# Kernel optimization log

Hardware: AMD Instinct MI355X
Metric: run time of the kernel (lower is better)

## Reference

```python
import jax, jax.numpy as jnp
import numpy as np

SOS = 1

def _gru_cell(x, h, Wih, Whh, bih, bhh):
    # PyTorch GRU cell: gates ordered (r, z, n)
    gi = x @ Wih.T + bih
    gh = h @ Whh.T + bhh
    ir, iz, inn = jnp.split(gi, 3, axis=-1)
    hr, hz, hn = jnp.split(gh, 3, axis=-1)
    r = jax.nn.sigmoid(ir + hr)
    z = jax.nn.sigmoid(iz + hz)
    n = jnp.tanh(inn + r * hn)
    return (1.0 - z) * n + z * h


def setup_inputs() -> dict:
    key = jax.random.key(0)
    ks = jax.random.split(key, 17)
    V, E, H, Lin, Tout, B, Lmax = 50000, 512, 512, 400, 100, 64, 400
    s = 0.05
    f = jax.random.normal
    return {
        "emb":     f(ks[0], (V, E)) * s,
        "enc_Wih": f(ks[1], (3 * H, E)) * s,
        "enc_Whh": f(ks[2], (3 * H, H)) * s,
        "enc_bih": f(ks[3], (3 * H,)) * s,
        "enc_bhh": f(ks[4], (3 * H,)) * s,
        "attn_W":  f(ks[5], (Lmax, 2 * H)) * s,
        "attn_b":  f(ks[6], (Lmax,)) * s,
        "comb_W":  f(ks[7], (H, 2 * H)) * s,
        "comb_b":  f(ks[8], (H,)) * s,
        "dec_Wih": f(ks[9], (3 * H, H)) * s,
        "dec_Whh": f(ks[10], (3 * H, H)) * s,
        "dec_bih": f(ks[11], (3 * H,)) * s,
        "dec_bhh": f(ks[12], (3 * H,)) * s,
        "out_W":   f(ks[13], (V, H)) * s,
        "out_b":   f(ks[14], (V,)) * s,
        "input_tensor":  jax.random.randint(ks[15], (Lin, B), 0, V),
        "target_tensor": jax.random.randint(ks[16], (Tout, B), 0, V),
    }


def reference(emb, enc_Wih, enc_Whh, enc_bih, enc_bhh, attn_W, attn_b,
              comb_W, comb_b, dec_Wih, dec_Whh, dec_bih, dec_bhh,
              out_W, out_b, input_tensor, target_tensor):
    B = input_tensor.shape[1]
    H = enc_Whh.shape[1]

    # ---- encoder: 1-layer GRU over [L, B, E] ----
    enc_x = emb[input_tensor]                      # [L, B, E]
    h0 = jnp.zeros((B, H), enc_x.dtype)
    def enc_step(h, x):
        h2 = _gru_cell(x, h, enc_Wih, enc_Whh, enc_bih, enc_bhh)
        return h2, h2
    h_enc, enc_out = jax.lax.scan(enc_step, h0, enc_x)   # enc_out: [L, B, H]
    enc0 = enc_out[0]                              # [B, H]; source's attn_applied[0] picks timestep 0

    # ---- decoder: teacher-forced, NLLLoss(mean) summed over steps ----
    dec_tokens = jnp.concatenate(
        [jnp.full((1, B), SOS, target_tensor.dtype), target_tensor[:-1]], axis=0)
    dec_x = emb[dec_tokens]                        # [T, B, H] (embed_size == hidden_size)

    def dec_step(h, xt):
        x, tgt = xt                                # x: [B, H], tgt: [B]
        a = jax.nn.softmax(jnp.concatenate([x, h], 1) @ attn_W.T + attn_b, axis=1)  # [B, Lmax]
        # faithful to source: elementwise broadcast picks enc_out[0] scaled by a[:, 0]
        ctx = enc0 * a[:, :1]                      # [B, H]
        c = jax.nn.relu(jnp.concatenate([x, ctx], 1) @ comb_W.T + comb_b)           # [B, H]
        h2 = _gru_cell(c, h, dec_Wih, dec_Whh, dec_bih, dec_bhh)
        logp = jax.nn.log_softmax(h2 @ out_W.T + out_b, axis=1)                     # [B, V]
        loss_t = -jnp.mean(jnp.take_along_axis(logp, tgt[:, None], axis=1))
        return h2, loss_t

    _, losses = jax.lax.scan(dec_step, h_enc, (dec_x, target_tensor))
    return jnp.sum(losses)
```

## Files before the change

### kernel.cpp

```cpp
#include <hip/hip_runtime.h>
#include <math.h>


typedef __attribute__((ext_vector_type(8))) short bh8;
typedef __attribute__((ext_vector_type(4))) float fv4;

__device__ __forceinline__ float b2f(short u) {
    union { unsigned int i; float f; } c;
    c.i = ((unsigned int)(unsigned short)u) << 16;
    return c.f;
}
__device__ __forceinline__ short f2b(float f) {
    union { float f; unsigned int u; } c;
    c.f = f;
    unsigned int r = (c.u + 0x7fffu + ((c.u >> 16) & 1u)) >> 16;
    return (short)r;
}
__device__ __forceinline__ bh8 ld8(const float* __restrict__ p) {
    bh8 r;
    #pragma unroll
    for (int j = 0; j < 8; ++j) r[j] = f2b(p[j]);
    return r;
}
__device__ __forceinline__ float sigmf(float x) { return 1.f / (1.f + expf(-x)); }

__device__ __forceinline__ fv4 mfma16(bh8 a, bh8 b, fv4 c) {
    return __builtin_amdgcn_mfma_f32_16x16x32_bf16(a, b, c, 0, 0, 0);
}

__device__ __forceinline__ void gridbar(unsigned int* bar, unsigned int target) {
    __syncthreads();
    if (threadIdx.x == 0) {
        __hip_atomic_fetch_add(bar, 1u, __ATOMIC_ACQ_REL, __HIP_MEMORY_SCOPE_AGENT);
        while (__hip_atomic_load(bar, __ATOMIC_ACQUIRE, __HIP_MEMORY_SCOPE_AGENT) < target) {
            __builtin_amdgcn_s_sleep(2);
        }
    }
    __syncthreads();
}

__global__ __launch_bounds__(256) void k_cvt(
    const float* __restrict__ s, short* __restrict__ d, int n)
{
    const int i = (blockIdx.x * 256 + threadIdx.x) * 4;
    if (i + 3 < n) {
        fv4 v = *(const fv4*)(s + i);
        short4 o;
        o.x = f2b(v[0]); o.y = f2b(v[1]); o.z = f2b(v[2]); o.w = f2b(v[3]);
        *(short4*)(d + i) = o;
    }
}

__global__ __launch_bounds__(256) void k_enc_persist(
    const float* __restrict__ emb, const int* __restrict__ input_t,
    const short* __restrict__ Wb,
    const float* __restrict__ Wih_f, const float* __restrict__ Whh_f,
    const float* __restrict__ bih, const float* __restrict__ bhh,
    float* __restrict__ h_f32, short* __restrict__ h_bf,
    float* __restrict__ enc0, unsigned int* __restrict__ bar)
{
    const int tid  = threadIdx.x;
    const int lane = tid & 63;
    const int wv   = tid >> 6;
    const int n0   = blockIdx.x * 16;
    const int b0   = wv * 16;
    const int l15  = lane & 15;
    const int ko   = lane >> 4;
    const int koff = ko * 8;
    const int brow = b0 + l15;
    const int n    = n0 + l15;

    for (int i = blockIdx.x * 256 + tid; i < 64 * 512; i += 32 * 256) {
        h_f32[i] = 0.f; h_bf[i] = 0;
    }
    gridbar(bar, 32u);

    const bh8 *Wrb = nullptr, *Wzb = nullptr, *Wnb = nullptr;
    const bh8 *Urb = nullptr, *Uzb = nullptr, *Unb = nullptr;
    const float *Wrf = nullptr, *Wzf = nullptr, *Wnf = nullptr;
    const float *Urf = nullptr, *Uzf = nullptr, *Unf = nullptr;
    if (Wb) {
        Wrb = (const bh8*)(Wb + (long long)(n + 0)    * 512) + ko;
        Wzb = (const bh8*)(Wb + (long long)(n + 512)  * 512) + ko;
        Wnb = (const bh8*)(Wb + (long long)(n + 1024) * 512) + ko;
        Urb = (const bh8*)(Wb + (long long)(n + 1536) * 512) + ko;
        Uzb = (const bh8*)(Wb + (long long)(n + 2048) * 512) + ko;
        Unb = (const bh8*)(Wb + (long long)(n + 2560) * 512) + ko;
    } else {
        Wrf = Wih_f + (long long)(n + 0)    * 512 + koff;
        Wzf = Wih_f + (long long)(n + 512)  * 512 + koff;
        Wnf = Wih_f + (long long)(n + 1024) * 512 + koff;
        Urf = Whh_f + (long long)(n + 0)    * 512 + koff;
        Uzf = Whh_f + (long long)(n + 512)  * 512 + koff;
        Unf = Whh_f + (long long)(n + 1024) * 512 + koff;
    }
    const float bir = bih[n], biz = bih[n + 512], bin = bih[n + 1024];
    const float bhr = bhh[n], bhz = bhh[n + 512], bhn = bhh[n + 1024];

    for (int t = 0; t < 400; ++t) {
        const float* hi  = h_f32 + (t & 1) * 32768;
        const short* hib = h_bf  + (t & 1) * 32768;
        float* ho  = h_f32 + ((t + 1) & 1) * 32768;
        short* hob = h_bf  + ((t + 1) & 1) * 32768;

        const int tok = input_t[t * 64 + brow];
        const float* Ap = emb + (long long)tok * 512 + koff;
        const bh8*  Hp  = (const bh8*)(hib + (long long)brow * 512) + ko;

        fv4 air = {0.f, 0.f, 0.f, 0.f};
        fv4 aiz = air, ain = air, ahr = air, ahz = air, ahn = air;
        if (Wb) {
            #pragma unroll 4
            for (int kk = 0; kk < 16; ++kk) {
                const bh8 a = ld8(Ap + kk * 32);
                const bh8 h = Hp[kk * 4];
                air = mfma16(a, Wrb[kk * 4], air);
                aiz = mfma16(a, Wzb[kk * 4], aiz);
                ain = mfma16(a, Wnb[kk * 4], ain);
                ahr = mfma16(h, Urb[kk * 4], ahr);
                ahz = mfma16(h, Uzb[kk * 4], ahz);
                ahn = mfma16(h, Unb[kk * 4], ahn);
            }
        } else {
            #pragma unroll 4
            for (int kk = 0; kk < 16; ++kk) {
                const bh8 a = ld8(Ap + kk * 32);
                const bh8 h = Hp[kk * 4];
                air = mfma16(a, ld8(Wrf + kk * 32), air);
                aiz = mfma16(a, ld8(Wzf + kk * 32), aiz);
                ain = mfma16(a, ld8(Wnf + kk * 32), ain);
                ahr = mfma16(h, ld8(Urf + kk * 32), ahr);
                ahz = mfma16(h, ld8(Uzf + kk * 32), ahz);
                ahn = mfma16(h, ld8(Unf + kk * 32), ahn);
            }
        }
        #pragma unroll
        for (int r = 0; r < 4; ++r) {
            const int b = b0 + ko * 4 + r;
            const float rr = sigmf(air[r] + bir + ahr[r] + bhr);
            const float zz = sigmf(aiz[r] + biz + ahz[r] + bhz);
            const float nn = tanhf(ain[r] + bin + rr * (ahn[r] + bhn));
            const float hold = hi[b * 512 + n];
            const float hnew = (1.f - zz) * nn + zz * hold;
            ho[b * 512 + n] = hnew;
            hob[b * 512 + n] = f2b(hnew);
            if (t == 0) enc0[b * 512 + n] = hnew;
        }
        gridbar(bar, 32u * (t + 2));
    }
}

__global__ __launch_bounds__(256) void k_gru1(
    const short* __restrict__ c_bf, const short* __restrict__ Wb,
    const float* __restrict__ Wih_f, const float* __restrict__ Whh_f,
    const float* __restrict__ bih, const float* __restrict__ bhh,
    const float* __restrict__ hi, const short* __restrict__ hib,
    float* __restrict__ ho, short* __restrict__ hob)
{
    const int tid  = threadIdx.x;
    const int lane = tid & 63;
    const int w    = blockIdx.x * 4 + (tid >> 6);
    const int b0   = (w & 3) * 16;
    const int n0   = (w >> 2) * 16;
    const int l15  = lane & 15;
    const int ko   = lane >> 4;
    const int koff = ko * 8;
    const int brow = b0 + l15;
    const int n    = n0 + l15;

    const bh8* Ap = (const bh8*)(c_bf + (long long)brow * 512) + ko;
    const bh8* Hp = (const bh8*)(hib + (long long)brow * 512) + ko;

    fv4 air = {0.f, 0.f, 0.f, 0.f};
    fv4 aiz = air, ain = air, ahr = air, ahz = air, ahn = air;
    if (Wb) {
        const bh8* Wr = (const bh8*)(Wb + (long long)(n + 0)    * 512) + ko;
        const bh8* Wz = (const bh8*)(Wb + (long long)(n + 512)  * 512) + ko;
        const bh8* Wn = (const bh8*)(Wb + (long long)(n + 1024) * 512) + ko;
        const bh8* Ur = (const bh8*)(Wb + (long long)(n + 1536) * 512) + ko;
        const bh8* Uz = (const bh8*)(Wb + (long long)(n + 2048) * 512) + ko;
        const bh8* Un = (const bh8*)(Wb + (long long)(n + 2560) * 512) + ko;
        #pragma unroll 4
        for (int kk = 0; kk < 16; ++kk) {
            const bh8 a = Ap[kk * 4];
            const bh8 h = Hp[kk * 4];
            air = mfma16(a, Wr[kk * 4], air);
            aiz = mfma16(a, Wz[kk * 4], aiz);
            ain = mfma16(a, Wn[kk * 4], ain);
            ahr = mfma16(h, Ur[kk * 4], ahr);
            ahz = mfma16(h, Uz[kk * 4], ahz);
            ahn = mfma16(h, Un[kk * 4], ahn);
        }
    } else {
        const float* Wr = Wih_f + (long long)(n + 0)    * 512 + koff;
        const float* Wz = Wih_f + (long long)(n + 512)  * 512 + koff;
        const float* Wn = Wih_f + (long long)(n + 1024) * 512 + koff;
        const float* Ur = Whh_f + (long long)(n + 0)    * 512 + koff;
        const float* Uz = Whh_f + (long long)(n + 512)  * 512 + koff;
        const float* Un = Whh_f + (long long)(n + 1024) * 512 + koff;
        #pragma unroll 4
        for (int kk = 0; kk < 16; ++kk) {
            const bh8 a = Ap[kk * 4];
            const bh8 h = Hp[kk * 4];
            air = mfma16(a, ld8(Wr + kk * 32), air);
            aiz = mfma16(a, ld8(Wz + kk * 32), aiz);
            ain = mfma16(a, ld8(Wn + kk * 32), ain);
            ahr = mfma16(h, ld8(Ur + kk * 32), ahr);
            ahz = mfma16(h, ld8(Uz + kk * 32), ahz);
            ahn = mfma16(h, ld8(Un + kk * 32), ahn);
        }
    }
    const float bir = bih[n], biz = bih[n + 512], bin = bih[n + 1024];
    const float bhr = bhh[n], bhz = bhh[n + 512], bhn = bhh[n + 1024];
    #pragma unroll
    for (int r = 0; r < 4; ++r) {
        const int b = b0 + ko * 4 + r;
        const float rr = sigmf(air[r] + bir + ahr[r] + bhr);
        const float zz = sigmf(aiz[r] + biz + ahz[r] + bhz);
        const float nn = tanhf(ain[r] + bin + rr * (ahn[r] + bhn));
        const float hold = hi[b * 512 + n];
        const float hnew = (1.f - zz) * nn + zz * hold;
        ho[b * 512 + n] = hnew;
        hob[b * 512 + n] = f2b(hnew);
    }
}

__global__ __launch_bounds__(256) void k_attncomb(
    const float* __restrict__ emb, const float* __restrict__ h_f32,
    const float* __restrict__ enc0,
    const float* __restrict__ attn_W, const float* __restrict__ attn_b,
    const float* __restrict__ comb_W, const float* __restrict__ comb_b,
    const int* __restrict__ target, int td, short* __restrict__ c_bf)
{
    __shared__ float sx[1024];
    __shared__ float sc[400];
    __shared__ float red[256];
    __shared__ float a0s;
    const int b = blockIdx.x;
    const int tid = threadIdx.x;
    const int tok = (td == 0) ? 1 : target[(td - 1) * 64 + b];
    for (int k = tid; k < 512; k += 256) {
        sx[k] = emb[(long long)tok * 512 + k];
        sx[512 + k] = h_f32[b * 512 + k];
    }
    __syncthreads();
    for (int nn = tid; nn < 400; nn += 256) {
        const fv4* wrow = (const fv4*)(attn_W + (long long)nn * 1024);
        float acc = 0.f;
        for (int kc = 0; kc < 256; ++kc) {
            fv4 v = wrow[kc];
            acc += v[0] * sx[kc * 4 + 0] + v[1] * sx[kc * 4 + 1]
                 + v[2] * sx[kc * 4 + 2] + v[3] * sx[kc * 4 + 3];
        }
        sc[nn] = acc + attn_b[nn];
    }
    __syncthreads();
    float m = -1e30f;
    for (int nn = tid; nn < 400; nn += 256) m = fmaxf(m, sc[nn]);
    red[tid] = m;
    __syncthreads();
    for (int s = 128; s > 0; s >>= 1) {
        if (tid < s) red[tid] = fmaxf(red[tid], red[tid + s]);
        __syncthreads();
    }
    m = red[0];
    __syncthreads();
    float ss = 0.f;
    for (int nn = tid; nn < 400; nn += 256) ss += expf(sc[nn] - m);
    red[tid] = ss;
    __syncthreads();
    for (int s = 128; s > 0; s >>= 1) {
        if (tid < s) red[tid] += red[tid + s];
        __syncthreads();
    }
    if (tid == 0) a0s = expf(sc[0] - m) / red[0];
    __syncthreads();
    const float a0b = a0s;
    for (int k = tid; k < 512; k += 256) sx[512 + k] = enc0[b * 512 + k] * a0b;
    __syncthreads();
    for (int j = tid; j < 512; j += 256) {
        const fv4* wrow = (const fv4*)(comb_W + (long long)j * 1024);
        float acc = 0.f;
        for (int kc = 0; kc < 256; ++kc) {
            fv4 v = wrow[kc];
            acc += v[0] * sx[kc * 4 + 0] + v[1] * sx[kc * 4 + 1]
                 + v[2] * sx[kc * 4 + 2] + v[3] * sx[kc * 4 + 3];
        }
        acc += comb_b[j];
        c_bf[b * 512 + j] = f2b(fmaxf(acc, 0.f));
    }
}

__global__ __launch_bounds__(256) void k_outloss(
    const short* __restrict__ h2bf,
    const short* __restrict__ outWb, const float* __restrict__ outW,
    const float* __restrict__ outb, const int* __restrict__ target,
    float* __restrict__ pm, float* __restrict__ ps, float* __restrict__ tlogit)
{
    __shared__ float sl[64][65];
    const int tid  = threadIdx.x;
    const int lane = tid & 63;
    const int wl   = tid >> 6;
    const int base = blockIdx.x * 64;
    const int n0   = base + wl * 16;
    const int l15  = lane & 15;
    const int ko   = lane >> 4;

    const int v    = n0 + l15;
    const int vcl  = (v < 50000) ? v : 49999;
    const bh8* A0 = (const bh8*)(h2bf + (long long)(0  + l15) * 512) + ko;
    const bh8* A1 = (const bh8*)(h2bf + (long long)(16 + l15) * 512) + ko;
    const bh8* A2 = (const bh8*)(h2bf + (long long)(32 + l15) * 512) + ko;
    const bh8* A3 = (const bh8*)(h2bf + (long long)(48 + l15) * 512) + ko;
    fv4 c0 = {0.f, 0.f, 0.f, 0.f};
    fv4 c1 = c0, c2 = c0, c3 = c0;
    if (outWb) {
        const bh8* Bp = (const bh8*)(outWb + (long long)vcl * 512) + ko;
        #pragma unroll 4
        for (int kk = 0; kk < 16; ++kk) {
            const bh8 bb = Bp[kk * 4];
            c0 = mfma16(A0[kk * 4], bb, c0);
            c1 = mfma16(A1[kk * 4], bb, c1);
            c2 = mfma16(A2[kk * 4], bb, c2);
            c3 = mfma16(A3[kk * 4], bb, c3);
        }
    } else {
        const float* Bp = outW + (long long)vcl * 512 + ko * 8;
        #pragma unroll 4
        for (int kk = 0; kk < 16; ++kk) {
            const bh8 bb = ld8(Bp + kk * 32);
            c0 = mfma16(A0[kk * 4], bb, c0);
            c1 = mfma16(A1[kk * 4], bb, c1);
            c2 = mfma16(A2[kk * 4], bb, c2);
            c3 = mfma16(A3[kk * 4], bb, c3);
        }
    }
    const float bv = outb[vcl];
    const int cc = wl * 16 + l15;
    const bool ok = (v < 50000);
    #pragma unroll
    for (int r = 0; r < 4; ++r) {
        const int row = ko * 4 + r;
        sl[0  + row][cc] = ok ? (c0[r] + bv) : -1e30f;
        sl[16 + row][cc] = ok ? (c1[r] + bv) : -1e30f;
        sl[32 + row][cc] = ok ? (c2[r] + bv) : -1e30f;
        sl[48 + row][cc] = ok ? (c3[r] + bv) : -1e30f;
    }
    __syncthreads();
    if (tid < 64) {
        const int b = tid;
        float m = -1e30f, s = 0.f;
        for (int c = 0; c < 64; ++c) {
            const float x = sl[b][c];
            if (x > m) { s = s * expf(m - x) + 1.f; m = x; }
            else       { s += expf(x - m); }
        }
        pm[blockIdx.x * 64 + b] = m;
        ps[blockIdx.x * 64 + b] = s;
        const int tg = target[b];
        const int rel = tg - base;
        if (rel >= 0 && rel < 64) tlogit[b] = sl[b][rel];
    }
}

__global__ __launch_bounds__(256) void k_lossred(
    const float* __restrict__ pm, const float* __restrict__ ps,
    const float* __restrict__ tlogit, float* __restrict__ loss_acc)
{
    __shared__ float rm[256], rs[256];
    const int b = blockIdx.x;
    const int tid = threadIdx.x;
    float m = -1e30f, s = 0.f;
    for (int i = tid; i < 782; i += 256) {
        const float m2 = pm[i * 64 + b];
        const float s2 = ps[i * 64 + b];
        if (m2 > m) { s = s * expf(m - m2) + s2; m = m2; }
        else        { s += s2 * expf(m2 - m); }
    }
    rm[tid] = m; rs[tid] = s;
    __syncthreads();
    for (int st = 128; st > 0; st >>= 1) {
        if (tid < st) {
            const float m2 = rm[tid + st], s2 = rs[tid + st];
            const float M = fmaxf(rm[tid], m2);
            rs[tid] = rs[tid] * expf(rm[tid] - M) + s2 * expf(m2 - M);
            rm[tid] = M;
        }
        __syncthreads();
    }
    if (tid == 0) {
        const float logp = tlogit[b] - (rm[0] + logf(rs[0]));
        atomicAdd(loss_acc, -logp * (1.f / 64.f));
    }
}

__global__ void k_init(float* h_f32_0, short* h_bf_0, float* loss_acc,
                       unsigned int* bar)
{
    const int i = blockIdx.x * 256 + threadIdx.x;
    if (i < 64 * 512) { h_f32_0[i] = 0.f; h_bf_0[i] = 0; }
    if (i == 0) { *loss_acc = 0.f; *bar = 0u; }
}

__global__ void k_final(const float* loss_acc, float* out)
{
    out[0] = *loss_acc;
}

extern "C" void kernel_launch(void* const* d_in, const int* in_sizes, int n_in,
                              void* d_out, int out_size, void* d_ws, size_t ws_size,
                              hipStream_t stream)
{
    const float* emb     = (const float*)d_in[0];
    const float* enc_Wih = (const float*)d_in[1];
    const float* enc_Whh = (const float*)d_in[2];
    const float* enc_bih = (const float*)d_in[3];
    const float* enc_bhh = (const float*)d_in[4];
    const float* attn_W  = (const float*)d_in[5];
    const float* attn_b  = (const float*)d_in[6];
    const float* comb_W  = (const float*)d_in[7];
    const float* comb_b  = (const float*)d_in[8];
    const float* dec_Wih = (const float*)d_in[9];
    const float* dec_Whh = (const float*)d_in[10];
    const float* dec_bih = (const float*)d_in[11];
    const float* dec_bhh = (const float*)d_in[12];
    const float* out_W   = (const float*)d_in[13];
    const float* out_b   = (const float*)d_in[14];
    const int*   input_t = (const int*)d_in[15];
    const int*   target_t= (const int*)d_in[16];

    char* ws = (char*)d_ws;
    float* h_f32  = (float*)(ws + 0);
    float* enc0   = (float*)(ws + 262144);
    short* h_bf   = (short*)(ws + 393216);
    short* c_bf   = (short*)(ws + 524288);
    float* lacc   = (float*)(ws + 589824);
    unsigned int* bar = (unsigned int*)(ws + 590080);
    float* pm     = (float*)(ws + 590336);
    float* ps     = (float*)(ws + 790528);
    float* tlog   = (float*)(ws + 990720);
    short* encWb  = (short*)(ws + 990976);
    short* decWb  = (short*)(ws + 4136704);
    short* outWb  = (short*)(ws + 7282432);

    const bool tier1 = ws_size >= 7282432;
    const bool tier2 = ws_size >= 58482432;

    k_init<<<128, 256, 0, stream>>>(h_f32, h_bf, lacc, bar);

    if (tier1) {
        k_cvt<<<768, 256, 0, stream>>>(enc_Wih, encWb, 786432);
        k_cvt<<<768, 256, 0, stream>>>(enc_Whh, encWb + 786432, 786432);
        k_cvt<<<768, 256, 0, stream>>>(dec_Wih, decWb, 786432);
        k_cvt<<<768, 256, 0, stream>>>(dec_Whh, decWb + 786432, 786432);
    }
    if (tier2) {
        k_cvt<<<25000, 256, 0, stream>>>(out_W, outWb, 25600000);
    }

    k_enc_persist<<<32, 256, 0, stream>>>(
        emb, input_t, tier1 ? encWb : nullptr, enc_Wih, enc_Whh,
        enc_bih, enc_bhh, h_f32, h_bf, enc0, bar);

    for (int td = 0; td < 100; ++td) {
        const float* hi  = h_f32 + (td & 1) * 32768;
        const short* hib = h_bf  + (td & 1) * 32768;
        float* ho  = h_f32 + ((td + 1) & 1) * 32768;
        short* hob = h_bf  + ((td + 1) & 1) * 32768;
        k_attncomb<<<64, 256, 0, stream>>>(emb, hi, enc0, attn_W, attn_b,
                                           comb_W, comb_b, target_t, td, c_bf);
        k_gru1<<<32, 256, 0, stream>>>(c_bf, tier1 ? decWb : nullptr,
                                       dec_Wih, dec_Whh, dec_bih, dec_bhh,
                                       hi, hib, ho, hob);
        k_outloss<<<782, 256, 0, stream>>>(hob, tier2 ? outWb : nullptr, out_W,
                                           out_b, target_t + td * 64,
                                           pm, ps, tlog);
        k_lossred<<<64, 256, 0, stream>>>(pm, ps, tlog, lacc);
    }

    k_final<<<1, 1, 0, stream>>>(lacc, (float*)d_out);
}
```

Measured before the change: 28.92 ms.

## Fuse whole encoder-decoder pipeline into one persistent megakernel with grid barriers

Replaces the conversion kernels, the persistent encoder kernel and the roughly 400 per-step decoder kernel launches with a single 256-block persistent kernel. Stages are separated by software grid barriers: a dedicated barrier counter for the 32 encoder blocks and a global one for the other phases. The aim is to remove launch overhead and inter-kernel gaps across the 100 decoder steps. In exchange it relies on all 256 blocks being co-resident for the spin barriers and adds barrier latency on every phase.

```diff
diff --git a/kernel.cpp b/kernel.cpp
--- a/kernel.cpp
+++ b/kernel.cpp
@@ -5,14 +5,8 @@
 typedef __attribute__((ext_vector_type(8))) short bh8;
 typedef __attribute__((ext_vector_type(4))) float fv4;
 
-__device__ __forceinline__ float b2f(short u) {
-    union { unsigned int i; float f; } c;
-    c.i = ((unsigned int)(unsigned short)u) << 16;
-    return c.f;
-}
 __device__ __forceinline__ short f2b(float f) {
-    union { float f; unsigned int u; } c;
-    c.f = f;
+    union { float f; unsigned int u; } c; c.f = f;
     unsigned int r = (c.u + 0x7fffu + ((c.u >> 16) & 1u)) >> 16;
     return (short)r;
 }
@@ -23,388 +17,396 @@
     return r;
 }
 __device__ __forceinline__ float sigmf(float x) { return 1.f / (1.f + expf(-x)); }
-
 __device__ __forceinline__ fv4 mfma16(bh8 a, bh8 b, fv4 c) {
     return __builtin_amdgcn_mfma_f32_16x16x32_bf16(a, b, c, 0, 0, 0);
 }
 
-__device__ __forceinline__ void gridbar(unsigned int* bar, unsigned int target) {
+__device__ __forceinline__ void spinbar(unsigned int* bar, unsigned int target) {
     __syncthreads();
     if (threadIdx.x == 0) {
         __hip_atomic_fetch_add(bar, 1u, __ATOMIC_ACQ_REL, __HIP_MEMORY_SCOPE_AGENT);
-        while (__hip_atomic_load(bar, __ATOMIC_ACQUIRE, __HIP_MEMORY_SCOPE_AGENT) < target) {
+        while (__hip_atomic_load(bar, __ATOMIC_ACQUIRE, __HIP_MEMORY_SCOPE_AGENT) < target)
+            __builtin_amdgcn_s_sleep(8);
+    }
+    __syncthreads();
+}
+__device__ __forceinline__ void spinbar2(unsigned int* bar, unsigned int target) {
+    __syncthreads();
+    if (threadIdx.x == 0) {
+        __hip_atomic_fetch_add(bar, 1u, __ATOMIC_ACQ_REL, __HIP_MEMORY_SCOPE_AGENT);
+        while (__hip_atomic_load(bar, __ATOMIC_ACQUIRE, __HIP_MEMORY_SCOPE_AGENT) < target)
             __builtin_amdgcn_s_sleep(2);
-        }
     }
     __syncthreads();
 }
 
-__global__ __launch_bounds__(256) void k_cvt(
-    const float* __restrict__ s, short* __restrict__ d, int n)
-{
-    const int i = (blockIdx.x * 256 + threadIdx.x) * 4;
-    if (i + 3 < n) {
+__device__ __forceinline__ void cvtbuf(const float* __restrict__ s,
+                                       short* __restrict__ d, int n, int gtid) {
+    for (int i = gtid * 4; i < n; i += 65536 * 4) {
         fv4 v = *(const fv4*)(s + i);
-        short4 o;
-        o.x = f2b(v[0]); o.y = f2b(v[1]); o.z = f2b(v[2]); o.w = f2b(v[3]);
+        short4 o; o.x = f2b(v[0]); o.y = f2b(v[1]); o.z = f2b(v[2]); o.w = f2b(v[3]);
         *(short4*)(d + i) = o;
     }
 }
 
-__global__ __launch_bounds__(256) void k_enc_persist(
-    const float* __restrict__ emb, const int* __restrict__ input_t,
-    const short* __restrict__ Wb,
-    const float* __restrict__ Wih_f, const float* __restrict__ Whh_f,
-    const float* __restrict__ bih, const float* __restrict__ bhh,
+__global__ void k_init(float* lacc, unsigned int* gbar, unsigned int* ebar) {
+    *lacc = 0.f; *gbar = 0u; *ebar = 0u;
+}
+
+__global__ __launch_bounds__(256, 1) void k_mega(
+    const float* __restrict__ emb,
+    const float* __restrict__ encWih, const float* __restrict__ encWhh,
+    const float* __restrict__ encbih, const float* __restrict__ encbhh,
+    const float* __restrict__ attnW,  const float* __restrict__ attnb,
+    const float* __restrict__ combW,  const float* __restrict__ combb,
+    const float* __restrict__ decWih, const float* __restrict__ decWhh,
+    const float* __restrict__ decbih, const float* __restrict__ decbhh,
+    const float* __restrict__ outW,   const float* __restrict__ outb,
+    const int* __restrict__ input_t,  const int* __restrict__ target_t,
     float* __restrict__ h_f32, short* __restrict__ h_bf,
-    float* __restrict__ enc0, unsigned int* __restrict__ bar)
-{
-    const int tid  = threadIdx.x;
-    const int lane = tid & 63;
-    const int wv   = tid >> 6;
-    const int n0   = blockIdx.x * 16;
-    const int b0   = wv * 16;
-    const int l15  = lane & 15;
-    const int ko   = lane >> 4;
-    const int koff = ko * 8;
-    const int brow = b0 + l15;
-    const int n    = n0 + l15;
-
-    for (int i = blockIdx.x * 256 + tid; i < 64 * 512; i += 32 * 256) {
-        h_f32[i] = 0.f; h_bf[i] = 0;
-    }
-    gridbar(bar, 32u);
-
-    const bh8 *Wrb = nullptr, *Wzb = nullptr, *Wnb = nullptr;
-    const bh8 *Urb = nullptr, *Uzb = nullptr, *Unb = nullptr;
-    const float *Wrf = nullptr, *Wzf = nullptr, *Wnf = nullptr;
-    const float *Urf = nullptr, *Uzf = nullptr, *Unf = nullptr;
-    if (Wb) {
-        Wrb = (const bh8*)(Wb + (long long)(n + 0)    * 512) + ko;
-        Wzb = (const bh8*)(Wb + (long long)(n + 512)  * 512) + ko;
-        Wnb = (const bh8*)(Wb + (long long)(n + 1024) * 512) + ko;
-        Urb = (const bh8*)(Wb + (long long)(n + 1536) * 512) + ko;
-        Uzb = (const bh8*)(Wb + (long long)(n + 2048) * 512) + ko;
-        Unb = (const bh8*)(Wb + (long long)(n + 2560) * 512) + ko;
-    } else {
-        Wrf = Wih_f + (long long)(n + 0)    * 512 + koff;
-        Wzf = Wih_f + (long long)(n + 512)  * 512 + koff;
-        Wnf = Wih_f + (long long)(n + 1024) * 512 + koff;
-        Urf = Whh_f + (long long)(n + 0)    * 512 + koff;
-        Uzf = Whh_f + (long long)(n + 512)  * 512 + koff;
-        Unf = Whh_f + (long long)(n + 1024) * 512 + koff;
-    }
-    const float bir = bih[n], biz = bih[n + 512], bin = bih[n + 1024];
-    const float bhr = bhh[n], bhz = bhh[n + 512], bhn = bhh[n + 1024];
-
-    for (int t = 0; t < 400; ++t) {
-        const float* hi  = h_f32 + (t & 1) * 32768;
-        const short* hib = h_bf  + (t & 1) * 32768;
-        float* ho  = h_f32 + ((t + 1) & 1) * 32768;
-        short* hob = h_bf  + ((t + 1) & 1) * 32768;
-
-        const int tok = input_t[t * 64 + brow];
-        const float* Ap = emb + (long long)tok * 512 + koff;
-        const bh8*  Hp  = (const bh8*)(hib + (long long)brow * 512) + ko;
-
-        fv4 air = {0.f, 0.f, 0.f, 0.f};
-        fv4 aiz = air, ain = air, ahr = air, ahz = air, ahn = air;
-        if (Wb) {
-            #pragma unroll 4
-            for (int kk = 0; kk < 16; ++kk) {
-                const bh8 a = ld8(Ap + kk * 32);
-                const bh8 h = Hp[kk * 4];
-                air = mfma16(a, Wrb[kk * 4], air);
-                aiz = mfma16(a, Wzb[kk * 4], aiz);
-                ain = mfma16(a, Wnb[kk * 4], ain);
-                ahr = mfma16(h, Urb[kk * 4], ahr);
-                ahz = mfma16(h, Uzb[kk * 4], ahz);
-                ahn = mfma16(h, Unb[kk * 4], ahn);
-            }
-        } else {
-            #pragma unroll 4
-            for (int kk = 0; kk < 16; ++kk) {
-                const bh8 a = ld8(Ap + kk * 32);
-                const bh8 h = Hp[kk * 4];
-                air = mfma16(a, ld8(Wrf + kk * 32), air);
-                aiz = mfma16(a, ld8(Wzf + kk * 32), aiz);
-                ain = mfma16(a, ld8(Wnf + kk * 32), ain);
-                ahr = mfma16(h, ld8(Urf + kk * 32), ahr);
-                ahz = mfma16(h, ld8(Uzf + kk * 32), ahz);
-                ahn = mfma16(h, ld8(Unf + kk * 32), ahn);
-            }
-        }
-        #pragma unroll
-        for (int r = 0; r < 4; ++r) {
-            const int b = b0 + ko * 4 + r;
-            const float rr = sigmf(air[r] + bir + ahr[r] + bhr);
-            const float zz = sigmf(aiz[r] + biz + ahz[r] + bhz);
-            const float nn = tanhf(ain[r] + bin + rr * (ahn[r] + bhn));
-            const float hold = hi[b * 512 + n];
-            const float hnew = (1.f - zz) * nn + zz * hold;
-            ho[b * 512 + n] = hnew;
-            hob[b * 512 + n] = f2b(hnew);
-            if (t == 0) enc0[b * 512 + n] = hnew;
-        }
-        gridbar(bar, 32u * (t + 2));
-    }
-}
-
-__global__ __launch_bounds__(256) void k_gru1(
-    const short* __restrict__ c_bf, const short* __restrict__ Wb,
-    const float* __restrict__ Wih_f, const float* __restrict__ Whh_f,
-    const float* __restrict__ bih, const float* __restrict__ bhh,
-    const float* __restrict__ hi, const short* __restrict__ hib,
-    float* __restrict__ ho, short* __restrict__ hob)
-{
-    const int tid  = threadIdx.x;
-    const int lane = tid & 63;
-    const int w    = blockIdx.x * 4 + (tid >> 6);
-    const int b0   = (w & 3) * 16;
-    const int n0   = (w >> 2) * 16;
-    const int l15  = lane & 15;
-    const int ko   = lane >> 4;
-    const int koff = ko * 8;
-    const int brow = b0 + l15;
-    const int n    = n0 + l15;
-
-    const bh8* Ap = (const bh8*)(c_bf + (long long)brow * 512) + ko;
-    const bh8* Hp = (const bh8*)(hib + (long long)brow * 512) + ko;
-
-    fv4 air = {0.f, 0.f, 0.f, 0.f};
-    fv4 aiz = air, ain = air, ahr = air, ahz = air, ahn = air;
-    if (Wb) {
-        const bh8* Wr = (const bh8*)(Wb + (long long)(n + 0)    * 512) + ko;
-        const bh8* Wz = (const bh8*)(Wb + (long long)(n + 512)  * 512) + ko;
-        const bh8* Wn = (const bh8*)(Wb + (long long)(n + 1024) * 512) + ko;
-        const bh8* Ur = (const bh8*)(Wb + (long long)(n + 1536) * 512) + ko;
-        const bh8* Uz = (const bh8*)(Wb + (long long)(n + 2048) * 512) + ko;
-        const bh8* Un = (const bh8*)(Wb + (long long)(n + 2560) * 512) + ko;
-        #pragma unroll 4
-        for (int kk = 0; kk < 16; ++kk) {
-            const bh8 a = Ap[kk * 4];
-            const bh8 h = Hp[kk * 4];
-            air = mfma16(a, Wr[kk * 4], air);
-            aiz = mfma16(a, Wz[kk * 4], aiz);
-            ain = mfma16(a, Wn[kk * 4], ain);
-            ahr = mfma16(h, Ur[kk * 4], ahr);
-            ahz = mfma16(h, Uz[kk * 4], ahz);
-            ahn = mfma16(h, Un[kk * 4], ahn);
-        }
-    } else {
-        const float* Wr = Wih_f + (long long)(n + 0)    * 512 + koff;
-        const float* Wz = Wih_f + (long long)(n + 512)  * 512 + koff;
-        const float* Wn = Wih_f + (long long)(n + 1024) * 512 + koff;
-        const float* Ur = Whh_f + (long long)(n + 0)    * 512 + koff;
-        const float* Uz = Whh_f + (long long)(n + 512)  * 512 + koff;
-        const float* Un = Whh_f + (long long)(n + 1024) * 512 + koff;
-        #pragma unroll 4
-        for (int kk = 0; kk < 16; ++kk) {
-            const bh8 a = Ap[kk * 4];
-            const bh8 h = Hp[kk * 4];
-            air = mfma16(a, ld8(Wr + kk * 32), air);
-            aiz = mfma16(a, ld8(Wz + kk * 32), aiz);
-            ain = mfma16(a, ld8(Wn + kk * 32), ain);
-            ahr = mfma16(h, ld8(Ur + kk * 32), ahr);
-            ahz = mfma16(h, ld8(Uz + kk * 32), ahz);
-            ahn = mfma16(h, ld8(Un + kk * 32), ahn);
-        }
-    }
-    const float bir = bih[n], biz = bih[n + 512], bin = bih[n + 1024];
-    const float bhr = bhh[n], bhz = bhh[n + 512], bhn = bhh[n + 1024];
-    #pragma unroll
-    for (int r = 0; r < 4; ++r) {
-        const int b = b0 + ko * 4 + r;
-        const float rr = sigmf(air[r] + bir + ahr[r] + bhr);
-        const float zz = sigmf(aiz[r] + biz + ahz[r] + bhz);
-        const float nn = tanhf(ain[r] + bin + rr * (ahn[r] + bhn));
-        const float hold = hi[b * 512 + n];
-        const float hnew = (1.f - zz) * nn + zz * hold;
-        ho[b * 512 + n] = hnew;
-        hob[b * 512 + n] = f2b(hnew);
-    }
-}
-
-__global__ __launch_bounds__(256) void k_attncomb(
-    const float* __restrict__ emb, const float* __restrict__ h_f32,
-    const float* __restrict__ enc0,
-    const float* __restrict__ attn_W, const float* __restrict__ attn_b,
-    const float* __restrict__ comb_W, const float* __restrict__ comb_b,
-    const int* __restrict__ target, int td, short* __restrict__ c_bf)
+    float* __restrict__ enc0, short* __restrict__ c_bf,
+    float* __restrict__ pm, float* __restrict__ ps, float* __restrict__ tlog,
+    float* __restrict__ lacc, unsigned int* __restrict__ gbar,
+    unsigned int* __restrict__ ebar,
+    short* __restrict__ encWb, short* __restrict__ decWb,
+    short* __restrict__ outWb, int tier, float* __restrict__ outp)
 {
     __shared__ float sx[1024];
     __shared__ float sc[400];
     __shared__ float red[256];
+    __shared__ float rs2[256];
     __shared__ float a0s;
-    const int b = blockIdx.x;
+    __shared__ float sl[64][65];
+    __shared__ float sqm[256];
+    __shared__ float sqs[256];
+
+    const int bid = blockIdx.x;
     const int tid = threadIdx.x;
-    const int tok = (td == 0) ? 1 : target[(td - 1) * 64 + b];
-    for (int k = tid; k < 512; k += 256) {
-        sx[k] = emb[(long long)tok * 512 + k];
-        sx[512 + k] = h_f32[b * 512 + k];
-    }
-    __syncthreads();
-    for (int nn = tid; nn < 400; nn += 256) {
-        const fv4* wrow = (const fv4*)(attn_W + (long long)nn * 1024);
-        float acc = 0.f;
-        for (int kc = 0; kc < 256; ++kc) {
-            fv4 v = wrow[kc];
-            acc += v[0] * sx[kc * 4 + 0] + v[1] * sx[kc * 4 + 1]
-                 + v[2] * sx[kc * 4 + 2] + v[3] * sx[kc * 4 + 3];
-        }
-        sc[nn] = acc + attn_b[nn];
-    }
-    __syncthreads();
-    float m = -1e30f;
-    for (int nn = tid; nn < 400; nn += 256) m = fmaxf(m, sc[nn]);
-    red[tid] = m;
-    __syncthreads();
-    for (int s = 128; s > 0; s >>= 1) {
-        if (tid < s) red[tid] = fmaxf(red[tid], red[tid + s]);
+    const int gtid = bid * 256 + tid;
+    unsigned int gc = 0;
+
+    if (gtid < 32768) { h_f32[gtid] = 0.f; h_bf[gtid] = 0; }
+    if (tier >= 1) {
+        cvtbuf(encWih, encWb, 786432, gtid);
+        cvtbuf(encWhh, encWb + 786432, 786432, gtid);
+        cvtbuf(decWih, decWb, 786432, gtid);
+        cvtbuf(decWhh, decWb + 786432, 786432, gtid);
+    }
+    if (tier >= 2) cvtbuf(outW, outWb, 25600000, gtid);
+    gc += 256; spinbar(gbar, gc);
+
+    if (bid < 32) {
+        const int wv = tid >> 6, lane = tid & 63;
+        const int l15 = lane & 15, ko = lane >> 4, koff = ko * 8;
+        const int n0 = bid * 16, b0 = wv * 16;
+        const int brow = b0 + l15, n = n0 + l15;
+        const float bir = encbih[n], biz = encbih[n + 512], bin = encbih[n + 1024];
+        const float bhr = encbhh[n], bhz = encbhh[n + 512], bhn = encbhh[n + 1024];
+        unsigned int ec = 0;
+        #pragma unroll 1
+        for (int t = 0; t < 400; ++t) {
+            const float* hi  = h_f32 + (t & 1) * 32768;
+            const short* hib = h_bf  + (t & 1) * 32768;
+            float* ho  = h_f32 + ((t + 1) & 1) * 32768;
+            short* hob = h_bf  + ((t + 1) & 1) * 32768;
+            const int tok = input_t[t * 64 + brow];
+            const float* Ap = emb + (long long)tok * 512 + koff;
+            const bh8*  Hp  = (const bh8*)(hib + (long long)brow * 512) + ko;
+            fv4 air = {0.f, 0.f, 0.f, 0.f};
+            fv4 aiz = air, ain = air, ahr = air, ahz = air, ahn = air;
+            if (tier >= 1) {
+                const bh8* Wr = (const bh8*)(encWb + (long long)(n + 0)    * 512) + ko;
+                const bh8* Wz = (const bh8*)(encWb + (long long)(n + 512)  * 512) + ko;
+                const bh8* Wn = (const bh8*)(encWb + (long long)(n + 1024) * 512) + ko;
+                const bh8* Ur = (const bh8*)(encWb + (long long)(n + 1536) * 512) + ko;
+                const bh8* Uz = (const bh8*)(encWb + (long long)(n + 2048) * 512) + ko;
+                const bh8* Un = (const bh8*)(encWb + (long long)(n + 2560) * 512) + ko;
+                #pragma unroll 4
+                for (int kk = 0; kk < 16; ++kk) {
+                    const bh8 a = ld8(Ap + kk * 32);
+                    const bh8 h = Hp[kk * 4];
+                    air = mfma16(a, Wr[kk * 4], air);
+                    aiz = mfma16(a, Wz[kk * 4], aiz);
+                    ain = mfma16(a, Wn[kk * 4], ain);
+                    ahr = mfma16(h, Ur[kk * 4], ahr);
+                    ahz = mfma16(h, Uz[kk * 4], ahz);
+                    ahn = mfma16(h, Un[kk * 4], ahn);
+                }
+            } else {
+                const float* Wr = encWih + (long long)(n + 0)    * 512 + koff;
+                const float* Wz = encWih + (long long)(n + 512)  * 512 + koff;
+                const float* Wn = encWih + (long long)(n + 1024) * 512 + koff;
+                const float* Ur = encWhh + (long long)(n + 0)    * 512 + koff;
+                const float* Uz = encWhh + (long long)(n + 512)  * 512 + koff;
+                const float* Un = encWhh + (long long)(n + 1024) * 512 + koff;
+                #pragma unroll 4
+                for (int kk = 0; kk < 16; ++kk) {
+                    const bh8 a = ld8(Ap + kk * 32);
+                    const bh8 h = Hp[kk * 4];
+                    air = mfma16(a, ld8(Wr + kk * 32), air);
+                    aiz = mfma16(a, ld8(Wz + kk * 32), aiz);
+                    ain = mfma16(a, ld8(Wn + kk * 32), ain);
+                    ahr = mfma16(h, ld8(Ur + kk * 32), ahr);
+                    ahz = mfma16(h, ld8(Uz + kk * 32), ahz);
+                    ahn = mfma16(h, ld8(Un + kk * 32), ahn);
+                }
+            }
+            #pragma unroll
+            for (int r = 0; r < 4; ++r) {
+                const int b = b0 + ko * 4 + r;
+                const float rr = sigmf(air[r] + bir + ahr[r] + bhr);
+                const float zz = sigmf(aiz[r] + biz + ahz[r] + bhz);
+                const float nn = tanhf(ain[r] + bin + rr * (ahn[r] + bhn));
+                const float hold = hi[b * 512 + n];
+                const float hnew = (1.f - zz) * nn + zz * hold;
+                ho[b * 512 + n] = hnew;
+                hob[b * 512 + n] = f2b(hnew);
+                if (t == 0) enc0[b * 512 + n] = hnew;
+            }
+            ec += 32; spinbar2(ebar, ec);
+        }
+    }
+    gc += 256; spinbar(gbar, gc);
+
+    #pragma unroll 1
+    for (int td = 0; td < 100; ++td) {
+        const float* hi  = h_f32 + (td & 1) * 32768;
+        const short* hib = h_bf  + (td & 1) * 32768;
+        float* ho  = h_f32 + ((td + 1) & 1) * 32768;
+        short* hob = h_bf  + ((td + 1) & 1) * 32768;
+
+        if (bid < 64) {
+            const int b = bid;
+            const int tok = (td == 0) ? 1 : target_t[(td - 1) * 64 + b];
+            for (int k = tid; k < 512; k += 256) {
+                sx[k] = emb[(long long)tok * 512 + k];
+                sx[512 + k] = hi[b * 512 + k];
+            }
+            __syncthreads();
+            for (int nn = tid; nn < 400; nn += 256) {
+                const fv4* wrow = (const fv4*)(attnW + (long long)nn * 1024);
+                float acc = 0.f;
+                for (int kc = 0; kc < 256; ++kc) {
+                    fv4 v = wrow[kc];
+                    acc += v[0] * sx[kc * 4 + 0] + v[1] * sx[kc * 4 + 1]
+                         + v[2] * sx[kc * 4 + 2] + v[3] * sx[kc * 4 + 3];
+                }
+                sc[nn] = acc + attnb[nn];
+            }
+            __syncthreads();
+            float m = -1e30f;
+            for (int nn = tid; nn < 400; nn += 256) m = fmaxf(m, sc[nn]);
+            red[tid] = m;
+            __syncthreads();
+            for (int s = 128; s > 0; s >>= 1) {
+                if (tid < s) red[tid] = fmaxf(red[tid], red[tid + s]);
+                __syncthreads();
+            }
+            m = red[0];
+            __syncthreads();
+            float ss = 0.f;
+            for (int nn = tid; nn < 400; nn += 256) ss += expf(sc[nn] - m);
+            red[tid] = ss;
+            __syncthreads();
+            for (int s = 128; s > 0; s >>= 1) {
+                if (tid < s) red[tid] += red[tid + s];
+                __syncthreads();
+            }
+            if (tid == 0) a0s = expf(sc[0] - m) / red[0];
+            __syncthreads();
+            const float a0b = a0s;
+            for (int k = tid; k < 512; k += 256)
+                sx[512 + k] = enc0[b * 512 + k] * a0b;
+            __syncthreads();
+            for (int j = tid; j < 512; j += 256) {
+                const fv4* wrow = (const fv4*)(combW + (long long)j * 1024);
+                float acc = 0.f;
+                for (int kc = 0; kc < 256; ++kc) {
+                    fv4 v = wrow[kc];
+                    acc += v[0] * sx[kc * 4 + 0] + v[1] * sx[kc * 4 + 1]
+                         + v[2] * sx[kc * 4 + 2] + v[3] * sx[kc * 4 + 3];
+                }
+                acc += combb[j];
+                c_bf[b * 512 + j] = f2b(fmaxf(acc, 0.f));
+            }
+        } else if (bid < 128 && td > 0) {
+            const int b = bid - 64;
+            red[tid] = pm[tid * 64 + b]; rs2[tid] = ps[tid * 64 + b];
+            __syncthreads();
+            for (int st = 128; st > 0; st >>= 1) {
+                if (tid < st) {
+                    const float m2 = red[tid + st], s2 = rs2[tid + st];
+                    const float M = fmaxf(red[tid], m2);
+                    rs2[tid] = rs2[tid] * expf(red[tid] - M) + s2 * expf(m2 - M);
+                    red[tid] = M;
+                }
+                __syncthreads();
+            }
+            if (tid == 0) {
+                const float logp = tlog[b] - (red[0] + logf(rs2[0]));
+                atomicAdd(lacc, -logp * (1.f / 64.f));
+            }
+        }
+        gc += 256; spinbar(gbar, gc);
+
+        if (bid < 32) {
+            const int lane = tid & 63;
+            const int w = bid * 4 + (tid >> 6);
+            const int b0 = (w & 3) * 16, n0 = (w >> 2) * 16;
+            const int l15 = lane & 15, ko = lane >> 4, koff = ko * 8;
+            const int brow = b0 + l15, n = n0 + l15;
+            const bh8* Ap = (const bh8*)(c_bf + (long long)brow * 512) + ko;
+            const bh8* Hp = (const bh8*)(hib + (long long)brow * 512) + ko;
+            fv4 air = {0.f, 0.f, 0.f, 0.f};
+            fv4 aiz = air, ain = air, ahr = air, ahz = air, ahn = air;
+            if (tier >= 1) {
+                const bh8* Wr = (const bh8*)(decWb + (long long)(n + 0)    * 512) + ko;
+                const bh8* Wz = (const bh8*)(decWb + (long long)(n + 512)  * 512) + ko;
+                const bh8* Wn = (const bh8*)(decWb + (long long)(n + 1024) * 512) + ko;
+                const bh8* Ur = (const bh8*)(decWb + (long long)(n + 1536) * 512) + ko;
+                const bh8* Uz = (const bh8*)(decWb + (long long)(n + 2048) * 512) + ko;
+                const bh8* Un = (const bh8*)(decWb + (long long)(n + 2560) * 512) + ko;
+                #pragma unroll 4
+                for (int kk = 0; kk < 16; ++kk) {
+                    const bh8 a = Ap[kk * 4];
+                    const bh8 h = Hp[kk * 4];
+                    air = mfma16(a, Wr[kk * 4], air);
+                    aiz = mfma16(a, Wz[kk * 4], aiz);
+                    ain = mfma16(a, Wn[kk * 4], ain);
+                    ahr = mfma16(h, Ur[kk * 4], ahr);
+                    ahz = mfma16(h, Uz[kk * 4], ahz);
+                    ahn = mfma16(h, Un[kk * 4], ahn);
+                }
+            } else {
+                const float* Wr = decWih + (long long)(n + 0)    * 512 + koff;
+                const float* Wz = decWih + (long long)(n + 512)  * 512 + koff;
+                const float* Wn = decWih + (long long)(n + 1024) * 512 + koff;
+                const float* Ur = decWhh + (long long)(n + 0)    * 512 + koff;
+                const float* Uz = decWhh + (long long)(n + 512)  * 512 + koff;
+                const float* Un = decWhh + (long long)(n + 1024) * 512 + koff;
+                #pragma unroll 4
+                for (int kk = 0; kk < 16; ++kk) {
+                    const bh8 a = Ap[kk * 4];
+                    const bh8 h = Hp[kk * 4];
+                    air = mfma16(a, ld8(Wr + kk * 32), air);
+                    aiz = mfma16(a, ld8(Wz + kk * 32), aiz);
+                    ain = mfma16(a, ld8(Wn + kk * 32), ain);
+                    ahr = mfma16(h, ld8(Ur + kk * 32), ahr);
+                    ahz = mfma16(h, ld8(Uz + kk * 32), ahz);
+                    ahn = mfma16(h, ld8(Un + kk * 32), ahn);
+                }
+            }
+            const float bir = decbih[n], biz = decbih[n + 512], bin = decbih[n + 1024];
+            const float bhr = decbhh[n], bhz = decbhh[n + 512], bhn = decbhh[n + 1024];
+            #pragma unroll
+            for (int r = 0; r < 4; ++r) {
+                const int b = b0 + ko * 4 + r;
+                const float rr = sigmf(air[r] + bir + ahr[r] + bhr);
+                const float zz = sigmf(aiz[r] + biz + ahz[r] + bhz);
+                const float nn = tanhf(ain[r] + bin + rr * (ahn[r] + bhn));
+                const float hold = hi[b * 512 + n];
+                const float hnew = (1.f - zz) * nn + zz * hold;
+                ho[b * 512 + n] = hnew;
+                hob[b * 512 + n] = f2b(hnew);
+            }
+        }
+        gc += 256; spinbar(gbar, gc);
+
+        {
+            const int wl = tid >> 6, lane = tid & 63;
+            const int l15 = lane & 15, ko = lane >> 4;
+            const bh8* A0 = (const bh8*)(hob + (long long)(0  + l15) * 512) + ko;
+            const bh8* A1 = (const bh8*)(hob + (long long)(16 + l15) * 512) + ko;
+            const bh8* A2 = (const bh8*)(hob + (long long)(32 + l15) * 512) + ko;
+            const bh8* A3 = (const bh8*)(hob + (long long)(48 + l15) * 512) + ko;
+            const int row = tid & 63, q = tid >> 6;
+            const int tg = target_t[td * 64 + row];
+            float qm = -1e30f, qs = 0.f;
+            #pragma unroll 1
+            for (int j = 0; j < 4; ++j) {
+                const int strip = bid * 4 + wl + 1024 * j;
+                const int v = strip * 16 + l15;
+                const int vcl = (v < 50000) ? v : 49999;
+                fv4 c0 = {0.f, 0.f, 0.f, 0.f};
+                fv4 c1 = c0, c2 = c0, c3 = c0;
+                if (tier >= 2) {
+                    const bh8* Bp = (const bh8*)(outWb + (long long)vcl * 512) + ko;
+                    #pragma unroll 4
+                    for (int kk = 0; kk < 16; ++kk) {
+                        const bh8 bb = Bp[kk * 4];
+                        c0 = mfma16(A0[kk * 4], bb, c0);
+                        c1 = mfma16(A1[kk * 4], bb, c1);
+                        c2 = mfma16(A2[kk * 4], bb, c2);
+                        c3 = mfma16(A3[kk * 4], bb, c3);
+                    }
+                } else {
+                    const float* Bp = outW + (long long)vcl * 512 + ko * 8;
+                    #pragma unroll 4
+                    for (int kk = 0; kk < 16; ++kk) {
+                        const bh8 bb = ld8(Bp + kk * 32);
+                        c0 = mfma16(A0[kk * 4], bb, c0);
+                        c1 = mfma16(A1[kk * 4], bb, c1);
+                        c2 = mfma16(A2[kk * 4], bb, c2);
+                        c3 = mfma16(A3[kk * 4], bb, c3);
+                    }
+                }
+                const float bv = outb[vcl];
+                const bool ok = (v < 50000);
+                const int cc = wl * 16 + l15;
+                #pragma unroll
+                for (int r = 0; r < 4; ++r) {
+                    const int rw = ko * 4 + r;
+                    sl[0  + rw][cc] = ok ? (c0[r] + bv) : -1e30f;
+                    sl[16 + rw][cc] = ok ? (c1[r] + bv) : -1e30f;
+                    sl[32 + rw][cc] = ok ? (c2[r] + bv) : -1e30f;
+                    sl[48 + rw][cc] = ok ? (c3[r] + bv) : -1e30f;
+                }
+                __syncthreads();
+                const int vb = (bid * 4 + q + 1024 * j) * 16;
+                for (int i = 0; i < 16; ++i) {
+                    const float x = sl[row][q * 16 + i];
+                    if (x > qm) { qs = qs * expf(qm - x) + 1.f; qm = x; }
+                    else        { qs += expf(x - qm); }
+                }
+                const int rel = tg - vb;
+                if (rel >= 0 && rel < 16) tlog[row] = sl[row][q * 16 + rel];
+                __syncthreads();
+            }
+            sqm[tid] = qm; sqs[tid] = qs;
+            __syncthreads();
+            if (tid < 64) {
+                float m = -1e30f, s = 0.f;
+                for (int q2 = 0; q2 < 4; ++q2) {
+                    const float m2 = sqm[q2 * 64 + tid], s2 = sqs[q2 * 64 + tid];
+                    if (m2 > m) { s = s * expf(m - m2) + s2; m = m2; }
+                    else        { s += s2 * expf(m2 - m); }
+                }
+                pm[bid * 64 + tid] = m; ps[bid * 64 + tid] = s;
+            }
+        }
+        gc += 256; spinbar(gbar, gc);
+    }
+
+    if (bid >= 64 && bid < 128) {
+        const int b = bid - 64;
+        red[tid] = pm[tid * 64 + b]; rs2[tid] = ps[tid * 64 + b];
         __syncthreads();
-    }
-    m = red[0];
-    __syncthreads();
-    float ss = 0.f;
-    for (int nn = tid; nn < 400; nn += 256) ss += expf(sc[nn] - m);
-    red[tid] = ss;
-    __syncthreads();
-    for (int s = 128; s > 0; s >>= 1) {
-        if (tid < s) red[tid] += red[tid + s];
-        __syncthreads();
-    }
-    if (tid == 0) a0s = expf(sc[0] - m) / red[0];
-    __syncthreads();
-    const float a0b = a0s;
-    for (int k = tid; k < 512; k += 256) sx[512 + k] = enc0[b * 512 + k] * a0b;
-    __syncthreads();
-    for (int j = tid; j < 512; j += 256) {
-        const fv4* wrow = (const fv4*)(comb_W + (long long)j * 1024);
-        float acc = 0.f;
-        for (int kc = 0; kc < 256; ++kc) {
-            fv4 v = wrow[kc];
-            acc += v[0] * sx[kc * 4 + 0] + v[1] * sx[kc * 4 + 1]
-                 + v[2] * sx[kc * 4 + 2] + v[3] * sx[kc * 4 + 3];
-        }
-        acc += comb_b[j];
-        c_bf[b * 512 + j] = f2b(fmaxf(acc, 0.f));
-    }
-}
-
-__global__ __launch_bounds__(256) void k_outloss(
-    const short* __restrict__ h2bf,
-    const short* __restrict__ outWb, const float* __restrict__ outW,
-    const float* __restrict__ outb, const int* __restrict__ target,
-    float* __restrict__ pm, float* __restrict__ ps, float* __restrict__ tlogit)
-{
-    __shared__ float sl[64][65];
-    const int tid  = threadIdx.x;
-    const int lane = tid & 63;
-    const int wl   = tid >> 6;
-    const int base = blockIdx.x * 64;
-    const int n0   = base + wl * 16;
-    const int l15  = lane & 15;
-    const int ko   = lane >> 4;
-
-    const int v    = n0 + l15;
-    const int vcl  = (v < 50000) ? v : 49999;
-    const bh8* A0 = (const bh8*)(h2bf + (long long)(0  + l15) * 512) + ko;
-    const bh8* A1 = (const bh8*)(h2bf + (long long)(16 + l15) * 512) + ko;
-    const bh8* A2 = (const bh8*)(h2bf + (long long)(32 + l15) * 512) + ko;
-    const bh8* A3 = (const bh8*)(h2bf + (long long)(48 + l15) * 512) + ko;
-    fv4 c0 = {0.f, 0.f, 0.f, 0.f};
-    fv4 c1 = c0, c2 = c0, c3 = c0;
-    if (outWb) {
-        const bh8* Bp = (const bh8*)(outWb + (long long)vcl * 512) + ko;
-        #pragma unroll 4
-        for (int kk = 0; kk < 16; ++kk) {
-            const bh8 bb = Bp[kk * 4];
-            c0 = mfma16(A0[kk * 4], bb, c0);
-            c1 = mfma16(A1[kk * 4], bb, c1);
-            c2 = mfma16(A2[kk * 4], bb, c2);
-            c3 = mfma16(A3[kk * 4], bb, c3);
-        }
-    } else {
-        const float* Bp = outW + (long long)vcl * 512 + ko * 8;
-        #pragma unroll 4
-        for (int kk = 0; kk < 16; ++kk) {
-            const bh8 bb = ld8(Bp + kk * 32);
-            c0 = mfma16(A0[kk * 4], bb, c0);
-            c1 = mfma16(A1[kk * 4], bb, c1);
-            c2 = mfma16(A2[kk * 4], bb, c2);
-            c3 = mfma16(A3[kk * 4], bb, c3);
-        }
-    }
-    const float bv = outb[vcl];
-    const int cc = wl * 16 + l15;
-    const bool ok = (v < 50000);
-    #pragma unroll
-    for (int r = 0; r < 4; ++r) {
-        const int row = ko * 4 + r;
-        sl[0  + row][cc] = ok ? (c0[r] + bv) : -1e30f;
-        sl[16 + row][cc] = ok ? (c1[r] + bv) : -1e30f;
-        sl[32 + row][cc] = ok ? (c2[r] + bv) : -1e30f;
-        sl[48 + row][cc] = ok ? (c3[r] + bv) : -1e30f;
-    }
-    __syncthreads();
-    if (tid < 64) {
-        const int b = tid;
-        float m = -1e30f, s = 0.f;
-        for (int c = 0; c < 64; ++c) {
-            const float x = sl[b][c];
-            if (x > m) { s = s * expf(m - x) + 1.f; m = x; }
-            else       { s += expf(x - m); }
-        }
-        pm[blockIdx.x * 64 + b] = m;
-        ps[blockIdx.x * 64 + b] = s;
-        const int tg = target[b];
-        const int rel = tg - base;
-        if (rel >= 0 && rel < 64) tlogit[b] = sl[b][rel];
-    }
-}
-
-__global__ __launch_bounds__(256) void k_lossred(
-    const float* __restrict__ pm, const float* __restrict__ ps,
-    const float* __restrict__ tlogit, float* __restrict__ loss_acc)
-{
-    __shared__ float rm[256], rs[256];
-    const int b = blockIdx.x;
-    const int tid = threadIdx.x;
-    float m = -1e30f, s = 0.f;
-    for (int i = tid; i < 782; i += 256) {
-        const float m2 = pm[i * 64 + b];
-        const float s2 = ps[i * 64 + b];
-        if (m2 > m) { s = s * expf(m - m2) + s2; m = m2; }
-        else        { s += s2 * expf(m2 - m); }
-    }
-    rm[tid] = m; rs[tid] = s;
-    __syncthreads();
-    for (int st = 128; st > 0; st >>= 1) {
-        if (tid < st) {
-            const float m2 = rm[tid + st], s2 = rs[tid + st];
-            const float M = fmaxf(rm[tid], m2);
-            rs[tid] = rs[tid] * expf(rm[tid] - M) + s2 * expf(m2 - M);
-            rm[tid] = M;
-        }
-        __syncthreads();
-    }
-    if (tid == 0) {
-        const float logp = tlogit[b] - (rm[0] + logf(rs[0]));
-        atomicAdd(loss_acc, -logp * (1.f / 64.f));
-    }
-}
-
-__global__ void k_init(float* h_f32_0, short* h_bf_0, float* loss_acc,
-                       unsigned int* bar)
-{
-    const int i = blockIdx.x * 256 + threadIdx.x;
-    if (i < 64 * 512) { h_f32_0[i] = 0.f; h_bf_0[i] = 0; }
-    if (i == 0) { *loss_acc = 0.f; *bar = 0u; }
-}
-
-__global__ void k_final(const float* loss_acc, float* out)
-{
-    out[0] = *loss_acc;
+        for (int st = 128; st > 0; st >>= 1) {
+            if (tid < st) {
+                const float m2 = red[tid + st], s2 = rs2[tid + st];
+                const float M = fmaxf(red[tid], m2);
+                rs2[tid] = rs2[tid] * expf(red[tid] - M) + s2 * expf(m2 - M);
+                red[tid] = M;
+            }
+            __syncthreads();
+        }
+        if (tid == 0) {
+            const float logp = tlog[b] - (red[0] + logf(rs2[0]));
+            atomicAdd(lacc, -logp * (1.f / 64.f));
+        }
+    }
+    gc += 256; spinbar(gbar, gc);
+    if (bid == 0 && tid == 0) outp[0] = *lacc;
 }
 
 extern "C" void kernel_launch(void* const* d_in, const int* in_sizes, int n_in,
@@ -430,53 +432,30 @@
     const int*   target_t= (const int*)d_in[16];
 
     char* ws = (char*)d_ws;
-    float* h_f32  = (float*)(ws + 0);
-    float* enc0   = (float*)(ws + 262144);
-    short* h_bf   = (short*)(ws + 393216);
-    short* c_bf   = (short*)(ws + 524288);
-    float* lacc   = (float*)(ws + 589824);
-    unsigned int* bar = (unsigned int*)(ws + 590080);
-    float* pm     = (float*)(ws + 590336);
-    float* ps     = (float*)(ws + 790528);
-    float* tlog   = (float*)(ws + 990720);
-    short* encWb  = (short*)(ws + 990976);
-    short* decWb  = (short*)(ws + 4136704);
-    short* outWb  = (short*)(ws + 7282432);
-
-    const bool tier1 = ws_size >= 7282432;
-    const bool tier2 = ws_size >= 58482432;
-
-    k_init<<<128, 256, 0, stream>>>(h_f32, h_bf, lacc, bar);
-
-    if (tier1) {
-        k_cvt<<<768, 256, 0, stream>>>(enc_Wih, encWb, 786432);
-        k_cvt<<<768, 256, 0, stream>>>(enc_Whh, encWb + 786432, 786432);
-        k_cvt<<<768, 256, 0, stream>>>(dec_Wih, decWb, 786432);
-        k_cvt<<<768, 256, 0, stream>>>(dec_Whh, decWb + 786432, 786432);
-    }
-    if (tier2) {
-        k_cvt<<<25000, 256, 0, stream>>>(out_W, outWb, 25600000);
-    }
-
-    k_enc_persist<<<32, 256, 0, stream>>>(
-        emb, input_t, tier1 ? encWb : nullptr, enc_Wih, enc_Whh,
-        enc_bih, enc_bhh, h_f32, h_bf, enc0, bar);
-
-    for (int td = 0; td < 100; ++td) {
-        const float* hi  = h_f32 + (td & 1) * 32768;
-        const short* hib = h_bf  + (td & 1) * 32768;
-        float* ho  = h_f32 + ((td + 1) & 1) * 32768;
-        short* hob = h_bf  + ((td + 1) & 1) * 32768;
-        k_attncomb<<<64, 256, 0, stream>>>(emb, hi, enc0, attn_W, attn_b,
-                                           comb_W, comb_b, target_t, td, c_bf);
-        k_gru1<<<32, 256, 0, stream>>>(c_bf, tier1 ? decWb : nullptr,
-                                       dec_Wih, dec_Whh, dec_bih, dec_bhh,
-                                       hi, hib, ho, hob);
-        k_outloss<<<782, 256, 0, stream>>>(hob, tier2 ? outWb : nullptr, out_W,
-                                           out_b, target_t + td * 64,
-                                           pm, ps, tlog);
-        k_lossred<<<64, 256, 0, stream>>>(pm, ps, tlog, lacc);
-    }
-
-    k_final<<<1, 1, 0, stream>>>(lacc, (float*)d_out);
-}
+    float* h_f32 = (float*)(ws + 0);
+    float* enc0  = (float*)(ws + 262144);
+    short* h_bf  = (short*)(ws + 393216);
+    short* c_bf  = (short*)(ws + 524288);
+    float* lacc  = (float*)(ws + 589824);
+    unsigned int* gbar = (unsigned int*)(ws + 593920);
+    unsigned int* ebar = (unsigned int*)(ws + 598016);
+    float* tlog  = (float*)(ws + 602112);
+    float* pm    = (float*)(ws + 602368);
+    float* ps    = (float*)(ws + 667904);
+    short* encWb = (short*)(ws + 733440);
+    short* decWb = (short*)(ws + 3879168);
+    short* outWb = (short*)(ws + 7024896);
+
+    int tier = 0;
+    if (ws_size >= 7024896)  tier = 1;
+    if (ws_size >= 58224896) tier = 2;
+
+    k_init<<<1, 1, 0, stream>>>(lacc, gbar, ebar);
+    k_mega<<<256, 256, 0, stream>>>(
+        emb, enc_Wih, enc_Whh, enc_bih, enc_bhh,
+        attn_W, attn_b, comb_W, comb_b,
+        dec_Wih, dec_Whh, dec_bih, dec_bhh,
+        out_W, out_b, input_t, target_t,
+        h_f32, h_bf, enc0, c_bf, pm, ps, tlog, lacc,
+        gbar, ebar, encWb, decWb, outWb, tier, (float*)d_out);
+}
```

Measured after the change: 98.29 ms. +239.9%, slower.
